# Kernel optimization log

Measured on AMD Instinct MI355X. Metric: run time of the kernel, lower is better.

The kernel has to match this reference:

```python
import jax, jax.numpy as jnp
import numpy as np

# CycleFC1w1a constants (from init_kwargs / gen_offset)
IN_CH = 384
KH, KW = 1, 7  # cycle kernel; actual conv weight is 1x1
START = (KH * KW) // 2  # 3


def _gen_offset_x(C):
    # kernel_size[0] == 1 branch: off_y = 0, off_x[i] = (i + START) % KW - KW // 2
    i = jnp.arange(C)
    return (i + START) % KW - KW // 2  # int32, values in [-3, 3]


def setup_inputs() -> dict:
    key = jax.random.key(0)
    k1, k2, k3 = jax.random.split(key, 3)
    x = jax.random.normal(k1, (64, IN_CH, 32, 32), dtype=jnp.float32)
    weight = jax.random.normal(k2, (IN_CH, IN_CH), dtype=jnp.float32) * 0.05  # [out_ch, in_ch]
    bias = jax.random.normal(k3, (IN_CH,), dtype=jnp.float32) * 0.01
    return {"x": x, "weight": weight, "bias": bias}


def reference(x, weight, bias):
    B, C, H, W = x.shape
    # BinaryQuantizer forward: sign()
    xb = jnp.sign(x)
    wb = jnp.sign(weight)  # [O, C]

    # Fixed per-channel integer horizontal offsets -> exact shifted gather
    off_x = _gen_offset_x(C)                                  # [C]
    cols = jnp.arange(W)[None, :] + off_x[:, None]            # [C, W] sample col = w + off
    valid = (cols >= 0) & (cols < W)                          # zero-pad out of bounds
    cols_c = jnp.clip(cols, 0, W - 1)
    # gather along width per channel: [B, C, H, W]
    g = jnp.take_along_axis(xb, cols_c[None, :, None, :], axis=3)
    g = g * valid[None, :, None, :].astype(x.dtype)

    # pointwise (1x1) channel-mixing conv
    out = jnp.einsum('bchw,oc->bohw', g, wb) + bias[None, :, None, None]
    return out
```

## Files before the change

### kernel.cpp

```cpp
#include <hip/hip_runtime.h>
#include <stdint.h>


#define IN_CH 384
#define HH 32
#define WW 32
#define BB 64
#define HR 4

constexpr uint64_t P7(int t) {
  uint64_t m = 0;
  for (int k = 0; k < 64; ++k)
    if (k % 7 == t) m |= (1ull << k);
  return m;
}
__device__ __constant__ uint64_t Pm[7] = {P7(0), P7(1), P7(2), P7(3), P7(4), P7(5), P7(6)};

__global__ __launch_bounds__(64) void cyc_prep(const float* __restrict__ wgt,
                                               const float* __restrict__ bias,
                                               uint64_t* __restrict__ wbg,
                                               float* __restrict__ bias2t) {
  const int o = blockIdx.x;
  const int lane = threadIdx.x;
  __shared__ uint64_t wb_sh[6];
#pragma unroll
  for (int j = 0; j < 6; ++j) {
    uint64_t m = __ballot(wgt[o * IN_CH + j * 64 + lane] < 0.0f);
    if (lane == 0) wb_sh[j] = m;
  }
  __syncthreads();
  if (lane < 6) wbg[o * 6 + lane] = wb_sh[lane];
  if (lane < WW) {
    const int w = lane;
    int nv = 0, corr = 0;
#pragma unroll
    for (int j = 0; j < 6; ++j) {
      uint64_t V = 0;
#pragma unroll
      for (int d = -3; d <= 3; ++d) {
        int wd = w + d;
        if (wd >= 0 && wd < WW) V |= Pm[(d - j + 14) % 7];
      }
      nv += __popcll(V);
      corr += __popcll(wb_sh[j] & ~V);
    }
    bias2t[w * IN_CH + o] = bias[o] + (float)nv + 2.0f * (float)corr;
  }
}

__global__ __launch_bounds__(768) void cyc_fused(const float* __restrict__ x,
                                                 const uint64_t* __restrict__ wbg,
                                                 const float* __restrict__ bias2t,
                                                 float* __restrict__ out) {
  __shared__ uint64_t sh_G[HR][WW][6];
  const int t = threadIdx.x;
  const int b = blockIdx.x >> 3;
  const int h0 = (blockIdx.x & 7) * HR;
  const int wave = t >> 6, lane = t & 63;

  {
    uint32_t* shw = (uint32_t*)sh_G;
    const int h = lane >> 5, wcol = lane & 31;
#pragma unroll
    for (int p = 0; p < 2; ++p) {
      const int tau = wave + p * 12;
      const int r = tau / 6, j = tau % 6;
      const int c = j * 64 + lane;
      const int off = ((c % 7 + 3) % 7) - 3;
      const uint32_t shr = (off > 0) ? (uint32_t)off : 0u;
      const uint32_t shl = (off < 0) ? (uint32_t)(-off) : 0u;
      const float4* xp = reinterpret_cast<const float4*>(
          x + (size_t)((b * IN_CH + c) * HH + h0 + r) * WW);
      uint32_t myw = 0;
#pragma unroll
      for (int i = 0; i < 8; ++i) {
        float4 v = xp[i];
        myw |= (v.x < 0.0f ? 1u : 0u) << (i * 4 + 0);
        myw |= (v.y < 0.0f ? 1u : 0u) << (i * 4 + 1);
        myw |= (v.z < 0.0f ? 1u : 0u) << (i * 4 + 2);
        myw |= (v.w < 0.0f ? 1u : 0u) << (i * 4 + 3);
      }
      uint32_t s = (myw >> shr) << shl;
      constexpr uint32_t Mt[5] = {0xFFFF0000u, 0xFF00FF00u, 0xF0F0F0F0u,
                                  0xCCCCCCCCu, 0xAAAAAAAAu};
#pragma unroll
      for (int stp = 0; stp < 5; ++stp) {
        const int js = 16 >> stp;
        const uint32_t M = Mt[stp];
        uint32_t y = __shfl_xor(s, js);
        s = (lane & js) ? ((s & M) | ((y >> js) & ~M))
                        : ((s & ~M) | ((y << js) & M));
      }
      shw[((r * WW + wcol) * 6 + j) * 2 + h] = s;
    }
  }
  __syncthreads();

  const int og = __builtin_amdgcn_readfirstlane(wave);
  const int w = lane & 31, r2 = lane >> 5;
  const ulonglong2* gv = reinterpret_cast<const ulonglong2*>(&sh_G[r2][w][0]);
  const ulonglong2 a0 = gv[0], a1 = gv[1], a2 = gv[2];
  const ulonglong2* hv = reinterpret_cast<const ulonglong2*>(&sh_G[2 + r2][w][0]);
  const ulonglong2 b0 = hv[0], b1 = hv[1], b2 = hv[2];
  const uint64_t gA0 = a0.x, gA1 = a0.y, gA2 = a1.x, gA3 = a1.y, gA4 = a2.x, gA5 = a2.y;
  const uint64_t gB0 = b0.x, gB1 = b0.y, gB2 = b1.x, gB3 = b1.y, gB4 = b2.x, gB5 = b2.y;

  const float4* bsrc = reinterpret_cast<const float4*>(bias2t + w * IN_CH + og * 32);
  const uint64_t* wp = wbg + (size_t)og * 32 * 6;
  float* opA = out + ((size_t)b * IN_CH + og * 32) * (HH * WW) + h0 * WW + lane;
  float* opB = opA + 2 * WW;

#pragma unroll
  for (int ot = 0; ot < 4; ++ot) {
    const float4 bb0 = bsrc[ot * 2 + 0];
    const float4 bb1 = bsrc[ot * 2 + 1];
    const float bbv[8] = {bb0.x, bb0.y, bb0.z, bb0.w,
                          bb1.x, bb1.y, bb1.z, bb1.w};
#pragma unroll
    for (int i = 0; i < 8; ++i) {
      const int oi = ot * 8 + i;
      const uint64_t w0 = wp[oi * 6 + 0], w1 = wp[oi * 6 + 1], w2 = wp[oi * 6 + 2];
      const uint64_t w3 = wp[oi * 6 + 3], w4 = wp[oi * 6 + 4], w5 = wp[oi * 6 + 5];
      int mmA = __popcll(gA0 ^ w0) + __popcll(gA1 ^ w1) + __popcll(gA2 ^ w2) +
                __popcll(gA3 ^ w3) + __popcll(gA4 ^ w4) + __popcll(gA5 ^ w5);
      int mmB = __popcll(gB0 ^ w0) + __popcll(gB1 ^ w1) + __popcll(gB2 ^ w2) +
                __popcll(gB3 ^ w3) + __popcll(gB4 ^ w4) + __popcll(gB5 ^ w5);
      opA[oi * (HH * WW)] = bbv[i] - 2.0f * (float)mmA;
      opB[oi * (HH * WW)] = bbv[i] - 2.0f * (float)mmB;
    }
  }
}

extern "C" void kernel_launch(void* const* d_in, const int* in_sizes, int n_in,
                              void* d_out, int out_size, void* d_ws, size_t ws_size,
                              hipStream_t stream) {
  const float* x = (const float*)d_in[0];
  const float* wgt = (const float*)d_in[1];
  const float* bias = (const float*)d_in[2];
  float* out = (float*)d_out;

  uint64_t* wbg = (uint64_t*)d_ws;
  float* bias2t = (float*)((char*)d_ws + 18432);

  cyc_prep<<<IN_CH, 64, 0, stream>>>(wgt, bias, wbg, bias2t);
  cyc_fused<<<BB * (HH / HR), 768, 0, stream>>>(x, wbg, bias2t, out);
}
```

Before: 196.9 us.

## Split output channels across blocks, pack full image into padded shared memory

```diff
diff --git a/kernel.cpp b/kernel.cpp
--- a/kernel.cpp
+++ b/kernel.cpp
@@ -6,7 +6,6 @@
 #define HH 32
 #define WW 32
 #define BB 64
-#define HR 4
 
 constexpr uint64_t P7(int t) {
   uint64_t m = 0;
@@ -19,7 +18,7 @@
 __global__ __launch_bounds__(64) void cyc_prep(const float* __restrict__ wgt,
                                                const float* __restrict__ bias,
                                                uint64_t* __restrict__ wbg,
-                                               float* __restrict__ bias2t) {
+                                               float* __restrict__ bias2w) {
   const int o = blockIdx.x;
   const int lane = threadIdx.x;
   __shared__ uint64_t wb_sh[6];
@@ -44,33 +43,34 @@
       nv += __popcll(V);
       corr += __popcll(wb_sh[j] & ~V);
     }
-    bias2t[w * IN_CH + o] = bias[o] + (float)nv + 2.0f * (float)corr;
+    bias2w[o * WW + w] = bias[o] + (float)nv + 2.0f * (float)corr;
   }
 }
 
 __global__ __launch_bounds__(768) void cyc_fused(const float* __restrict__ x,
                                                  const uint64_t* __restrict__ wbg,
-                                                 const float* __restrict__ bias2t,
+                                                 const float* __restrict__ bias2w,
                                                  float* __restrict__ out) {
-  __shared__ uint64_t sh_G[HR][WW][6];
+  __shared__ uint64_t sh_G[HH * WW * 7];
   const int t = threadIdx.x;
-  const int b = blockIdx.x >> 3;
-  const int h0 = (blockIdx.x & 7) * HR;
-  const int wave = t >> 6, lane = t & 63;
+  const int lane = t & 63, wave = t >> 6;
+  const int bid = blockIdx.x;
+  const int oq = bid & 7;
+  const int b = bid >> 3;
 
   {
     uint32_t* shw = (uint32_t*)sh_G;
-    const int h = lane >> 5, wcol = lane & 31;
-#pragma unroll
-    for (int p = 0; p < 2; ++p) {
-      const int tau = wave + p * 12;
+    const int wcol = lane & 31, hhalf = lane >> 5;
+#pragma unroll 2
+    for (int p = 0; p < 16; ++p) {
+      const int tau = wave * 16 + p;
       const int r = tau / 6, j = tau % 6;
       const int c = j * 64 + lane;
       const int off = ((c % 7 + 3) % 7) - 3;
       const uint32_t shr = (off > 0) ? (uint32_t)off : 0u;
       const uint32_t shl = (off < 0) ? (uint32_t)(-off) : 0u;
       const float4* xp = reinterpret_cast<const float4*>(
-          x + (size_t)((b * IN_CH + c) * HH + h0 + r) * WW);
+          x + (size_t)((b * IN_CH + c) * HH + r) * WW);
       uint32_t myw = 0;
 #pragma unroll
       for (int i = 0; i < 8; ++i) {
@@ -91,42 +91,37 @@
         s = (lane & js) ? ((s & M) | ((y >> js) & ~M))
                         : ((s & ~M) | ((y << js) & M));
       }
-      shw[((r * WW + wcol) * 6 + j) * 2 + h] = s;
+      shw[((r * WW + wcol) * 7 + j) * 2 + hhalf] = s;
     }
   }
   __syncthreads();
 
-  const int og = __builtin_amdgcn_readfirstlane(wave);
-  const int w = lane & 31, r2 = lane >> 5;
-  const ulonglong2* gv = reinterpret_cast<const ulonglong2*>(&sh_G[r2][w][0]);
-  const ulonglong2 a0 = gv[0], a1 = gv[1], a2 = gv[2];
-  const ulonglong2* hv = reinterpret_cast<const ulonglong2*>(&sh_G[2 + r2][w][0]);
-  const ulonglong2 b0 = hv[0], b1 = hv[1], b2 = hv[2];
-  const uint64_t gA0 = a0.x, gA1 = a0.y, gA2 = a1.x, gA3 = a1.y, gA4 = a2.x, gA5 = a2.y;
-  const uint64_t gB0 = b0.x, gB1 = b0.y, gB2 = b1.x, gB3 = b1.y, gB4 = b2.x, gB5 = b2.y;
+  const int wu = __builtin_amdgcn_readfirstlane(wave);
+  const int o0 = oq * 48 + wu * 4;
+  const uint64_t* wp = wbg + (size_t)o0 * 6;
+  uint64_t Wg[4][6];
+#pragma unroll
+  for (int oo = 0; oo < 4; ++oo)
+#pragma unroll
+    for (int j = 0; j < 6; ++j) Wg[oo][j] = wp[oo * 6 + j];
 
-  const float4* bsrc = reinterpret_cast<const float4*>(bias2t + w * IN_CH + og * 32);
-  const uint64_t* wp = wbg + (size_t)og * 32 * 6;
-  float* opA = out + ((size_t)b * IN_CH + og * 32) * (HH * WW) + h0 * WW + lane;
-  float* opB = opA + 2 * WW;
+  const int w = lane & 31;
+  float bs[4];
+#pragma unroll
+  for (int oo = 0; oo < 4; ++oo) bs[oo] = bias2w[(o0 + oo) * WW + w];
 
+  float* op = out + ((size_t)b * IN_CH + o0) * (HH * WW) + lane;
+#pragma unroll 2
+  for (int p = 0; p < 16; ++p) {
+    const uint64_t* gp = sh_G + (size_t)(64 * p + lane) * 7;
+    const uint64_t g0 = gp[0], g1 = gp[1], g2 = gp[2];
+    const uint64_t g3 = gp[3], g4 = gp[4], g5 = gp[5];
 #pragma unroll
-  for (int ot = 0; ot < 4; ++ot) {
-    const float4 bb0 = bsrc[ot * 2 + 0];
-    const float4 bb1 = bsrc[ot * 2 + 1];
-    const float bbv[8] = {bb0.x, bb0.y, bb0.z, bb0.w,
-                          bb1.x, bb1.y, bb1.z, bb1.w};
-#pragma unroll
-    for (int i = 0; i < 8; ++i) {
-      const int oi = ot * 8 + i;
-      const uint64_t w0 = wp[oi * 6 + 0], w1 = wp[oi * 6 + 1], w2 = wp[oi * 6 + 2];
-      const uint64_t w3 = wp[oi * 6 + 3], w4 = wp[oi * 6 + 4], w5 = wp[oi * 6 + 5];
-      int mmA = __popcll(gA0 ^ w0) + __popcll(gA1 ^ w1) + __popcll(gA2 ^ w2) +
-                __popcll(gA3 ^ w3) + __popcll(gA4 ^ w4) + __popcll(gA5 ^ w5);
-      int mmB = __popcll(gB0 ^ w0) + __popcll(gB1 ^ w1) + __popcll(gB2 ^ w2) +
-                __popcll(gB3 ^ w3) + __popcll(gB4 ^ w4) + __popcll(gB5 ^ w5);
-      opA[oi * (HH * WW)] = bbv[i] - 2.0f * (float)mmA;
-      opB[oi * (HH * WW)] = bbv[i] - 2.0f * (float)mmB;
+    for (int oo = 0; oo < 4; ++oo) {
+      int mm = __popcll(g0 ^ Wg[oo][0]) + __popcll(g1 ^ Wg[oo][1]) +
+               __popcll(g2 ^ Wg[oo][2]) + __popcll(g3 ^ Wg[oo][3]) +
+               __popcll(g4 ^ Wg[oo][4]) + __popcll(g5 ^ Wg[oo][5]);
+      op[oo * (HH * WW) + p * 64] = bs[oo] - 2.0f * (float)mm;
     }
   }
 }
@@ -140,8 +135,8 @@
   float* out = (float*)d_out;
 
   uint64_t* wbg = (uint64_t*)d_ws;
-  float* bias2t = (float*)((char*)d_ws + 18432);
+  float* bias2w = (float*)((char*)d_ws + 18432);
 
-  cyc_prep<<<IN_CH, 64, 0, stream>>>(wgt, bias, wbg, bias2t);
-  cyc_fused<<<BB * (HH / HR), 768, 0, stream>>>(x, wbg, bias2t, out);
+  cyc_prep<<<IN_CH, 64, 0, stream>>>(wgt, bias, wbg, bias2w);
+  cyc_fused<<<BB * 8, 768, 0, stream>>>(x, wbg, bias2w, out);
 }
```

Measured after the change: 275.8 us. 1.4x slower.
